# Optimization experiments

Hardware: AMD Instinct MI355X
Metric: run time of the kernel (lower is better)

## Reference

```python
import jax, jax.numpy as jnp
import numpy as np

N_EMBD = 1024
N_HEAD = 16
HEAD_DIM = N_EMBD // N_HEAD
NEG = -1e10


def setup_inputs() -> dict:
    key = jax.random.key(0)
    ks = jax.random.split(key, 5)
    B, T, C = 4, 2048, N_EMBD
    s = 0.02
    return {
        "x": jax.random.normal(ks[0], (B, T, C), dtype=jnp.float32),
        "w_attn": jax.random.normal(ks[1], (C, 3 * C), dtype=jnp.float32) * s,
        "b_attn": jnp.zeros((3 * C,), dtype=jnp.float32),
        "w_proj": jax.random.normal(ks[2], (C, C), dtype=jnp.float32) * s,
        "b_proj": jnp.zeros((C,), dtype=jnp.float32),
    }


def reference(x, w_attn, b_attn, w_proj, b_proj):
    B, T, C = x.shape
    H, D = N_HEAD, HEAD_DIM
    qkv = x @ w_attn + b_attn                      # [B,T,3C]
    q, k, v = jnp.split(qkv, 3, axis=-1)
    q = q.reshape(B, T, H, D).transpose(0, 2, 1, 3)  # [B,H,T,D]
    k = k.reshape(B, T, H, D).transpose(0, 2, 1, 3)
    v = v.reshape(B, T, H, D).transpose(0, 2, 1, 3)
    att = jnp.einsum("bhqd,bhkd->bhqk", q, k) / jnp.sqrt(jnp.float32(D))
    # additive causal mask: strictly-upper triangle gets -1e10 (as in torch source)
    mask = jnp.triu(jnp.full((T, T), NEG, dtype=att.dtype), k=1)
    att = jax.nn.softmax(att + mask, axis=-1)
    y = jnp.einsum("bhqk,bhkd->bhqd", att, v)      # [B,H,T,D]
    y = y.transpose(0, 2, 1, 3).reshape(B, T, C)
    return y @ w_proj + b_proj
```

## Files before the change

### kernel.cpp

```cpp
#include <hip/hip_runtime.h>
#include <hip/hip_bf16.h>

#define T_SEQ 2048
#define NE    1024
#define NH    16
#define HD    64
#define QKV_N 3072
#define MROWS 8192

typedef __attribute__((ext_vector_type(8))) short short8;
typedef __attribute__((ext_vector_type(4))) float f32x4;

__device__ __forceinline__ short f2bf(float f) {
  __hip_bfloat16 h = __float2bfloat16(f);
  return *reinterpret_cast<short*>(&h);
}
__device__ __forceinline__ float bfu2f(unsigned short u) {
  unsigned int t = (unsigned int)u << 16;
  return __builtin_bit_cast(float, t);
}

__global__ __launch_bounds__(256) void transpose_cvt(const float* __restrict__ src,
                                                     short* __restrict__ dst,
                                                     int K, int N) {
  __shared__ short tile[32][33];
  int bn = blockIdx.x * 32;
  int bk = blockIdx.y * 32;
  int tx = threadIdx.x;
  int ty = threadIdx.y;
#pragma unroll
  for (int i = 0; i < 32; i += 8)
    tile[ty + i][tx] = f2bf(src[(size_t)(bk + ty + i) * N + bn + tx]);
  __syncthreads();
#pragma unroll
  for (int i = 0; i < 32; i += 8)
    dst[(size_t)(bn + ty + i) * K + bk + tx] = tile[tx][ty + i];
}

template <bool AF32, bool OUTF32>
__global__ __launch_bounds__(256) void gemm_bt_bias(const void* __restrict__ Av,
                                                    const short* __restrict__ Bt,
                                                    const float* __restrict__ bias,
                                                    void* __restrict__ Co,
                                                    int M, int N, int K) {
  __shared__ __align__(16) short As[128 * 40];
  __shared__ __align__(16) short Bs[128 * 40];
  const int m0 = blockIdx.x * 128;
  const int n0 = blockIdx.y * 128;
  const int tid = threadIdx.x;
  const int w = tid >> 6, lane = tid & 63;
  const int L15 = lane & 15, quad = lane >> 4;
  const int wr = (w >> 1) * 64, wc = (w & 1) * 64;
  const int srow = tid >> 2;
  const int scol = (tid & 3) * 8;

  f32x4 acc[4][4] = {};

  const float* Af = (const float*)Av;
  const short* Ab = (const short*)Av;

  for (int k0 = 0; k0 < K; k0 += 32) {
    short8 a0, a1;
    if (AF32) {
      const float* p0 = Af + (size_t)(m0 + srow) * K + k0 + scol;
      const float* p1 = Af + (size_t)(m0 + 64 + srow) * K + k0 + scol;
      float4 x00 = *(const float4*)p0, x01 = *(const float4*)(p0 + 4);
      float4 x10 = *(const float4*)p1, x11 = *(const float4*)(p1 + 4);
      a0 = short8{f2bf(x00.x), f2bf(x00.y), f2bf(x00.z), f2bf(x00.w),
                  f2bf(x01.x), f2bf(x01.y), f2bf(x01.z), f2bf(x01.w)};
      a1 = short8{f2bf(x10.x), f2bf(x10.y), f2bf(x10.z), f2bf(x10.w),
                  f2bf(x11.x), f2bf(x11.y), f2bf(x11.z), f2bf(x11.w)};
    } else {
      a0 = *(const short8*)(Ab + (size_t)(m0 + srow) * K + k0 + scol);
      a1 = *(const short8*)(Ab + (size_t)(m0 + 64 + srow) * K + k0 + scol);
    }
    short8 b0 = *(const short8*)(Bt + (size_t)(n0 + srow) * K + k0 + scol);
    short8 b1 = *(const short8*)(Bt + (size_t)(n0 + 64 + srow) * K + k0 + scol);

    __syncthreads();
    *(short8*)&As[srow * 40 + scol] = a0;
    *(short8*)&As[(64 + srow) * 40 + scol] = a1;
    *(short8*)&Bs[srow * 40 + scol] = b0;
    *(short8*)&Bs[(64 + srow) * 40 + scol] = b1;
    __syncthreads();

    short8 af[4], bfr[4];
#pragma unroll
    for (int i = 0; i < 4; ++i)
      af[i] = *(const short8*)&As[(wr + i * 16 + L15) * 40 + quad * 8];
#pragma unroll
    for (int j = 0; j < 4; ++j)
      bfr[j] = *(const short8*)&Bs[(wc + j * 16 + L15) * 40 + quad * 8];
#pragma unroll
    for (int i = 0; i < 4; ++i)
#pragma unroll
      for (int j = 0; j < 4; ++j)
        acc[i][j] = __builtin_amdgcn_mfma_f32_16x16x32_bf16(af[i], bfr[j], acc[i][j], 0, 0, 0);
  }

  float bv[4];
#pragma unroll
  for (int j = 0; j < 4; ++j) bv[j] = bias[n0 + wc + j * 16 + L15];
#pragma unroll
  for (int i = 0; i < 4; ++i)
#pragma unroll
    for (int j = 0; j < 4; ++j)
#pragma unroll
      for (int r = 0; r < 4; ++r) {
        size_t row = (size_t)(m0 + wr + i * 16 + quad * 4 + r);
        int col = n0 + wc + j * 16 + L15;
        float v = acc[i][j][r] + bv[j];
        if (OUTF32)
          ((float*)Co)[row * N + col] = v;
        else
          ((short*)Co)[row * N + col] = f2bf(v);
      }
}

__global__ __launch_bounds__(256) void attn_flash(const short* __restrict__ qkv,
                                                  short* __restrict__ y) {
  const int bx = blockIdx.x;
  const int bh = blockIdx.y;
  const int b = bh >> 4, h = bh & 15;
  const short* base = qkv + (size_t)b * T_SEQ * QKV_N;
  const int tid = threadIdx.x;
  const int w = tid >> 6, lane = tid & 63;
  const int L15 = lane & 15, quad = lane >> 4;

  __shared__ __align__(16) short Ks[64 * 80];
  __shared__ __align__(16) short Vts[64 * 80];
  __shared__ __align__(16) short Ps[4][32 * 72];

  const short one = (short)0x3F80;
  const short8 vone = short8{one, one, one, one, one, one, one, one};

  const float cs = 0.18033688011112042f;

  const short* kbase = base + NE + h * HD;
  const short* vbase = base + 2 * NE + h * HD;

  const int skey = tid >> 3;
  const int sd0 = (tid & 7) * 8;
  const int dv0 = w * 8;

#pragma unroll 1
  for (int seg = 0; seg < 2; ++seg) {
    const int qt = seg == 0 ? (T_SEQ / 128 - 1 - bx) : bx;

    short8 qf[2][2];
#pragma unroll
    for (int qs = 0; qs < 2; ++qs) {
      const short* qp =
          base + (size_t)(qt * 128 + w * 32 + qs * 16 + L15) * QKV_N + h * HD + quad * 8;
      qf[qs][0] = *(const short8*)qp;
      qf[qs][1] = *(const short8*)(qp + 32);
    }

    f32x4 O[2][4] = {};
    f32x4 L[2] = {};

    uint4 kv0 = *(const uint4*)(kbase + (size_t)skey * QKV_N + sd0);
    uint4 kv1 = *(const uint4*)(kbase + (size_t)(32 + skey) * QKV_N + sd0);
    uint4 vv0 = *(const uint4*)(vbase + (size_t)lane * QKV_N + dv0);
    uint4 vv1 = *(const uint4*)(vbase + (size_t)lane * QKV_N + dv0 + 32);

    const int nkt = 2 * qt + 2;
    for (int kt = 0; kt < nkt; ++kt) {
      __syncthreads();
      *(uint4*)&Ks[skey * 80 + sd0] = kv0;
      *(uint4*)&Ks[(32 + skey) * 80 + sd0] = kv1;
      {
        const short* pv0 = (const short*)&vv0;
        const short* pv1 = (const short*)&vv1;
#pragma unroll
        for (int j = 0; j < 8; ++j) {
          Vts[(dv0 + j) * 80 + lane] = pv0[j];
          Vts[(32 + dv0 + j) * 80 + lane] = pv1[j];
        }
      }
      __syncthreads();

      if (kt < nkt - 1) {
        int nt = kt + 1;
        kv0 = *(const uint4*)(kbase + (size_t)(nt * 64 + skey) * QKV_N + sd0);
        kv1 = *(const uint4*)(kbase + (size_t)(nt * 64 + 32 + skey) * QKV_N + sd0);
        vv0 = *(const uint4*)(vbase + (size_t)(nt * 64 + lane) * QKV_N + dv0);
        vv1 = *(const uint4*)(vbase + (size_t)(nt * 64 + lane) * QKV_N + dv0 + 32);
      }

      f32x4 S[2][4] = {};
#pragma unroll
      for (int nb = 0; nb < 4; ++nb) {
        short8 kb0 = *(const short8*)&Ks[(nb * 16 + L15) * 80 + quad * 8];
        short8 kb1 = *(const short8*)&Ks[(nb * 16 + L15) * 80 + 32 + quad * 8];
#pragma unroll
        for (int qs = 0; qs < 2; ++qs) {
          S[qs][nb] = __builtin_amdgcn_mfma_f32_16x16x32_bf16(qf[qs][0], kb0, S[qs][nb], 0, 0, 0);
          S[qs][nb] = __builtin_amdgcn_mfma_f32_16x16x32_bf16(qf[qs][1], kb1, S[qs][nb], 0, 0, 0);
        }
      }

      if (kt >= nkt - 2) {
#pragma unroll
        for (int qs = 0; qs < 2; ++qs)
#pragma unroll
          for (int nb = 0; nb < 4; ++nb) {
            int kg = kt * 64 + nb * 16 + L15;
#pragma unroll
            for (int r = 0; r < 4; ++r) {
              int qg = qt * 128 + w * 32 + qs * 16 + quad * 4 + r;
              if (kg > qg) S[qs][nb][r] = -1e30f;
            }
          }
      }

      short* myP = &Ps[w][0];
#pragma unroll
      for (int qs = 0; qs < 2; ++qs)
#pragma unroll
        for (int nb = 0; nb < 4; ++nb)
#pragma unroll
          for (int r = 0; r < 4; ++r)
            myP[(qs * 16 + quad * 4 + r) * 72 + nb * 16 + L15] =
                f2bf(__builtin_amdgcn_exp2f(S[qs][nb][r] * cs));
      asm volatile("" ::: "memory");
      short8 pf[2][2];
#pragma unroll
      for (int qs = 0; qs < 2; ++qs) {
        pf[qs][0] = *(const short8*)&myP[(qs * 16 + L15) * 72 + quad * 8];
        pf[qs][1] = *(const short8*)&myP[(qs * 16 + L15) * 72 + 32 + quad * 8];
      }

#pragma unroll
      for (int nb = 0; nb < 4; ++nb) {
        short8 vf0 = *(const short8*)&Vts[(nb * 16 + L15) * 80 + quad * 8];
        short8 vf1 = *(const short8*)&Vts[(nb * 16 + L15) * 80 + 32 + quad * 8];
#pragma unroll
        for (int qs = 0; qs < 2; ++qs) {
          O[qs][nb] = __builtin_amdgcn_mfma_f32_16x16x32_bf16(pf[qs][0], vf0, O[qs][nb], 0, 0, 0);
          O[qs][nb] = __builtin_amdgcn_mfma_f32_16x16x32_bf16(pf[qs][1], vf1, O[qs][nb], 0, 0, 0);
        }
      }
#pragma unroll
      for (int qs = 0; qs < 2; ++qs) {
        L[qs] = __builtin_amdgcn_mfma_f32_16x16x32_bf16(pf[qs][0], vone, L[qs], 0, 0, 0);
        L[qs] = __builtin_amdgcn_mfma_f32_16x16x32_bf16(pf[qs][1], vone, L[qs], 0, 0, 0);
      }
    }

#pragma unroll
    for (int qs = 0; qs < 2; ++qs) {
      float inv[4];
#pragma unroll
      for (int r = 0; r < 4; ++r) inv[r] = 1.0f / L[qs][r];
#pragma unroll
      for (int nb = 0; nb < 4; ++nb)
#pragma unroll
        for (int r = 0; r < 4; ++r) {
          size_t row =
              (size_t)b * T_SEQ + (size_t)(qt * 128 + w * 32 + qs * 16 + quad * 4 + r);
          int col = h * HD + nb * 16 + L15;
          y[row * NE + col] = f2bf(O[qs][nb][r] * inv[r]);
        }
    }
  }
}

extern "C" void kernel_launch(void* const* d_in, const int* in_sizes, int n_in,
                              void* d_out, int out_size, void* d_ws, size_t ws_size,
                              hipStream_t stream) {
  (void)in_sizes; (void)n_in; (void)out_size; (void)ws_size;
  const float* x      = (const float*)d_in[0];
  const float* w_attn = (const float*)d_in[1];
  const float* b_attn = (const float*)d_in[2];
  const float* w_proj = (const float*)d_in[3];
  const float* b_proj = (const float*)d_in[4];
  float* out = (float*)d_out;

  short* qkv = (short*)d_ws;
  short* wT2 = qkv;
  short* wT1 = qkv + (size_t)MROWS * QKV_N;
  short* y   = wT1;

  transpose_cvt<<<dim3(QKV_N / 32, NE / 32), dim3(32, 8), 0, stream>>>(w_attn, wT1, NE, QKV_N);

  gemm_bt_bias<true, false><<<dim3(MROWS / 128, QKV_N / 128), 256, 0, stream>>>(
      x, wT1, b_attn, qkv, MROWS, QKV_N, NE);

  attn_flash<<<dim3(T_SEQ / 256, 64), 256, 0, stream>>>(qkv, y);

  transpose_cvt<<<dim3(NE / 32, NE / 32), dim3(32, 8), 0, stream>>>(w_proj, wT2, NE, NE);

  gemm_bt_bias<false, true><<<dim3(MROWS / 128, NE / 128), 256, 0, stream>>>(
      y, wT2, b_proj, out, MROWS, NE, NE);
}
```

Before: 273.3 us.

## Stage GEMM tiles via direct global-to-LDS loads with XOR swizzle

```diff
diff --git a/kernel.cpp b/kernel.cpp
--- a/kernel.cpp
+++ b/kernel.cpp
@@ -18,6 +18,12 @@
 __device__ __forceinline__ float bfu2f(unsigned short u) {
   unsigned int t = (unsigned int)u << 16;
   return __builtin_bit_cast(float, t);
+}
+
+__device__ __forceinline__ void lds16(const void* g, void* l) {
+  __builtin_amdgcn_global_load_lds(
+      (const __attribute__((address_space(1))) unsigned int*)g,
+      (__attribute__((address_space(3))) unsigned int*)l, 16, 0, 0);
 }
 
 __global__ __launch_bounds__(256) void transpose_cvt(const float* __restrict__ src,
@@ -43,16 +49,17 @@
                                                     const float* __restrict__ bias,
                                                     void* __restrict__ Co,
                                                     int M, int N, int K) {
-  __shared__ __align__(16) short As[128 * 40];
-  __shared__ __align__(16) short Bs[128 * 40];
+  __shared__ __align__(16) unsigned char AsRaw[AF32 ? 16384 : 8192];
+  __shared__ __align__(16) short Bs[128 * 32];
+  float* Asf = (float*)AsRaw;
+  short* Asb = (short*)AsRaw;
+
   const int m0 = blockIdx.x * 128;
   const int n0 = blockIdx.y * 128;
   const int tid = threadIdx.x;
   const int w = tid >> 6, lane = tid & 63;
   const int L15 = lane & 15, quad = lane >> 4;
   const int wr = (w >> 1) * 64, wc = (w & 1) * 64;
-  const int srow = tid >> 2;
-  const int scol = (tid & 3) * 8;
 
   f32x4 acc[4][4] = {};
 
@@ -60,37 +67,54 @@
   const short* Ab = (const short*)Av;
 
   for (int k0 = 0; k0 < K; k0 += 32) {
-    short8 a0, a1;
+    __syncthreads();
+
     if (AF32) {
-      const float* p0 = Af + (size_t)(m0 + srow) * K + k0 + scol;
-      const float* p1 = Af + (size_t)(m0 + 64 + srow) * K + k0 + scol;
-      float4 x00 = *(const float4*)p0, x01 = *(const float4*)(p0 + 4);
-      float4 x10 = *(const float4*)p1, x11 = *(const float4*)(p1 + 4);
-      a0 = short8{f2bf(x00.x), f2bf(x00.y), f2bf(x00.z), f2bf(x00.w),
-                  f2bf(x01.x), f2bf(x01.y), f2bf(x01.z), f2bf(x01.w)};
-      a1 = short8{f2bf(x10.x), f2bf(x10.y), f2bf(x10.z), f2bf(x10.w),
-                  f2bf(x11.x), f2bf(x11.y), f2bf(x11.z), f2bf(x11.w)};
+#pragma unroll
+      for (int p = 0; p < 4; ++p) {
+        int r = p * 32 + w * 8 + (lane >> 3);
+        int gl = (lane & 7) ^ (r & 7);
+        lds16(Af + (size_t)(m0 + r) * K + k0 + gl * 4,
+              (char*)AsRaw + p * 4096 + w * 1024);
+      }
     } else {
-      a0 = *(const short8*)(Ab + (size_t)(m0 + srow) * K + k0 + scol);
-      a1 = *(const short8*)(Ab + (size_t)(m0 + 64 + srow) * K + k0 + scol);
-    }
-    short8 b0 = *(const short8*)(Bt + (size_t)(n0 + srow) * K + k0 + scol);
-    short8 b1 = *(const short8*)(Bt + (size_t)(n0 + 64 + srow) * K + k0 + scol);
+#pragma unroll
+      for (int p = 0; p < 2; ++p) {
+        int r = p * 64 + w * 16 + (lane >> 2);
+        int gl = (lane & 3) ^ ((r >> 1) & 3);
+        lds16(Ab + (size_t)(m0 + r) * K + k0 + gl * 8,
+              (char*)AsRaw + p * 4096 + w * 1024);
+      }
+    }
+#pragma unroll
+    for (int p = 0; p < 2; ++p) {
+      int r = p * 64 + w * 16 + (lane >> 2);
+      int gl = (lane & 3) ^ ((r >> 1) & 3);
+      lds16(Bt + (size_t)(n0 + r) * K + k0 + gl * 8,
+            (char*)Bs + p * 4096 + w * 1024);
+    }
 
     __syncthreads();
-    *(short8*)&As[srow * 40 + scol] = a0;
-    *(short8*)&As[(64 + srow) * 40 + scol] = a1;
-    *(short8*)&Bs[srow * 40 + scol] = b0;
-    *(short8*)&Bs[(64 + srow) * 40 + scol] = b1;
-    __syncthreads();
 
     short8 af[4], bfr[4];
 #pragma unroll
-    for (int i = 0; i < 4; ++i)
-      af[i] = *(const short8*)&As[(wr + i * 16 + L15) * 40 + quad * 8];
-#pragma unroll
-    for (int j = 0; j < 4; ++j)
-      bfr[j] = *(const short8*)&Bs[(wc + j * 16 + L15) * 40 + quad * 8];
+    for (int i = 0; i < 4; ++i) {
+      int r = wr + i * 16 + L15;
+      if (AF32) {
+        const float* rowp = Asf + r * 32;
+        f32x4 fa = *(const f32x4*)(rowp + ((2 * quad + 0) ^ (r & 7)) * 4);
+        f32x4 fb = *(const f32x4*)(rowp + ((2 * quad + 1) ^ (r & 7)) * 4);
+        af[i] = short8{f2bf(fa.x), f2bf(fa.y), f2bf(fa.z), f2bf(fa.w),
+                       f2bf(fb.x), f2bf(fb.y), f2bf(fb.z), f2bf(fb.w)};
+      } else {
+        af[i] = *(const short8*)(Asb + r * 32 + (quad ^ ((r >> 1) & 3)) * 8);
+      }
+    }
+#pragma unroll
+    for (int j = 0; j < 4; ++j) {
+      int r = wc + j * 16 + L15;
+      bfr[j] = *(const short8*)(Bs + r * 32 + (quad ^ ((r >> 1) & 3)) * 8);
+    }
 #pragma unroll
     for (int i = 0; i < 4; ++i)
 #pragma unroll
```

After: 274.5 us. About the same (+0.4%).
